# Performance work log

Hardware: AMD Instinct MI355X
Metric: run time of the kernel (lower is better)

Reference implementation:

```python
import jax, jax.numpy as jnp
import numpy as np
import math

B, S, E = 16, 600, 300   # batch, seq_len, enc_len
H, NC = 512, 2           # hidden, classes
D = S * E                # archi[0] = 180000


def setup_inputs() -> dict:
    key = jax.random.key(0)
    ks = jax.random.split(key, 7)
    x = jax.random.normal(ks[0], (B, S, E), dtype=jnp.float32)
    y = jax.random.randint(ks[1], (B,), 0, NC)
    # neurons initialized to zeros (init_neurons)
    n0 = jnp.zeros((B, S, E), jnp.float32)
    n1 = jnp.zeros((B, H), jnp.float32)
    n2 = jnp.zeros((B, NC), jnp.float32)
    # Linear weights (torch layout: [out, in]), Kaiming-uniform-like scale 1/sqrt(fan_in)
    W0 = jax.random.uniform(ks[2], (E, E), jnp.float32, -1.0, 1.0) / math.sqrt(E)
    W1 = jax.random.uniform(ks[3], (H, D), jnp.float32, -1.0, 1.0) / math.sqrt(D)
    b1 = jax.random.uniform(ks[4], (H,), jnp.float32, -1.0, 1.0) / math.sqrt(D)
    W2 = jax.random.uniform(ks[5], (NC, H), jnp.float32, -1.0, 1.0) / math.sqrt(H)
    b2 = jax.random.uniform(ks[6], (NC,), jnp.float32, -1.0, 1.0) / math.sqrt(H)
    return dict(x=x, y=y, n0=n0, n1=n1, n2=n2, W0=W0, W1=W1, b1=b1, W2=W2, b2=b2, T=3)


def reference(x, y, n0, n1, n2, W0, W1, b1, W2, b2, T):
    # EqProp free-phase relaxation (beta = 0.0, forward default).
    # Analytic dPhi/dneurons replaces torch.autograd.grad:
    scale = 1.0 / math.sqrt(E)
    Wx = jnp.einsum('bse,fe->bsf', x, W0)  # synapses[0](x), constant across steps
    for _ in range(T):
        g0 = Wx + (n1 @ W1).reshape(B, S, E)              # dPhi/dn0
        g1 = n0.reshape(B, D) @ W1.T + b1 + n2 @ W2       # dPhi/dn1
        g2 = n1 @ W2.T + b2                               # dPhi/dn2 (beta=0)
        # hand-coded attention update for neuron 0: Q=g0, K=V=x
        attn = jax.nn.softmax(scale * jnp.einsum('bse,bte->bst', g0, x), axis=-1)
        n0 = jnp.einsum('bst,bte->bse', attn, x)
        n1 = jnp.tanh(g1)
        n2 = jnp.tanh(g2)
    return n0, n1, n2
```

## Files before the change

kernel.cpp:

```cpp
#include <hip/hip_runtime.h>
#include <math.h>

#define DD 180000L
#define HH 512
#define BB 16
#define SS 600
#define EE 300
#define SP 608
#define EP 320

typedef unsigned short u16;
typedef __attribute__((ext_vector_type(8))) __bf16 bf16x8;
typedef __attribute__((ext_vector_type(4))) float f32x4;

__device__ __forceinline__ u16 f2bf(float f) {
  union { float f; unsigned int u; } x; x.f = f;
  unsigned int r = (x.u + 0x7FFFu + ((x.u >> 16) & 1u)) >> 16;
  return (u16)r;
}

__global__ __launch_bounds__(256) void k_conv_x(const float* __restrict__ x,
                                                u16* __restrict__ xb, u16* __restrict__ xt) {
  __shared__ u16 tl[32][33];
  int b = blockIdx.z;
  int tt = blockIdx.x * 32, ee = blockIdx.y * 32;
  int lx = threadIdx.x & 31, ly = threadIdx.x >> 5;
#pragma unroll
  for (int i = 0; i < 4; ++i) {
    int t = tt + ly + i * 8, e = ee + lx;
    float v = (t < SS && e < EE) ? x[((long)b * SS + t) * EE + e] : 0.f;
    u16 h = f2bf(v);
    xb[((long)b * SP + t) * EP + e] = h;
    tl[ly + i * 8][lx] = h;
  }
  __syncthreads();
#pragma unroll
  for (int i = 0; i < 4; ++i) {
    int e = ee + ly + i * 8, t = tt + lx;
    xt[((long)b * EP + e) * SP + t] = tl[lx][ly + i * 8];
  }
}

__global__ __launch_bounds__(256) void k_conv_w0(const float* __restrict__ W0, u16* __restrict__ w0b) {
  int idx = blockIdx.x * 256 + threadIdx.x;
  int f = idx / EP, e = idx % EP;
  float v = (f < EE && e < EE) ? W0[f * EE + e] : 0.f;
  w0b[idx] = f2bf(v);
}

__global__ __launch_bounds__(256) void k_gemm_nt(
    const u16* __restrict__ A, int lda, long sA, int Arows,
    const u16* __restrict__ B, int ldb, long sB, int Brows,
    float* __restrict__ C, int ldc, long sC, int Mv, int Nv, int K,
    u16* __restrict__ Cb, int ldcb, long sCb) {
  int bz = blockIdx.z;
  int m0 = blockIdx.x * 64, n0 = blockIdx.y * 64;
  int lane = threadIdx.x & 63, wv = threadIdx.x >> 6;
  int wm = m0 + (wv >> 1) * 32, wn = n0 + (wv & 1) * 32;
  int q = lane >> 4, ln = lane & 15;
  const u16* Ab = A + (long)bz * sA;
  const u16* Bb = B + (long)bz * sB;
  long arow0 = (long)min(wm + ln, Arows - 1) * lda;
  long arow1 = (long)min(wm + 16 + ln, Arows - 1) * lda;
  long brow0 = (long)min(wn + ln, Brows - 1) * ldb;
  long brow1 = (long)min(wn + 16 + ln, Brows - 1) * ldb;
  f32x4 acc00 = {0.f,0.f,0.f,0.f}, acc01 = acc00, acc10 = acc00, acc11 = acc00;
  int ksteps = (K + 31) >> 5;
  for (int kk = 0; kk < ksteps; ++kk) {
    int k0 = kk * 32 + q * 8;
    bf16x8 a0 = *(const bf16x8*)(Ab + arow0 + k0);
    bf16x8 a1 = *(const bf16x8*)(Ab + arow1 + k0);
    bf16x8 b0 = *(const bf16x8*)(Bb + brow0 + k0);
    bf16x8 bv1 = *(const bf16x8*)(Bb + brow1 + k0);
    acc00 = __builtin_amdgcn_mfma_f32_16x16x32_bf16(a0, b0,  acc00, 0, 0, 0);
    acc01 = __builtin_amdgcn_mfma_f32_16x16x32_bf16(a0, bv1, acc01, 0, 0, 0);
    acc10 = __builtin_amdgcn_mfma_f32_16x16x32_bf16(a1, b0,  acc10, 0, 0, 0);
    acc11 = __builtin_amdgcn_mfma_f32_16x16x32_bf16(a1, bv1, acc11, 0, 0, 0);
  }
  float* Cp = C + (long)bz * sC;
  u16* Cbp = Cb ? (Cb + (long)bz * sCb) : (u16*)0;
#pragma unroll
  for (int sm = 0; sm < 2; ++sm) {
#pragma unroll
    for (int sn = 0; sn < 2; ++sn) {
      f32x4 acc = (sm == 0) ? ((sn == 0) ? acc00 : acc01) : ((sn == 0) ? acc10 : acc11);
#pragma unroll
      for (int r = 0; r < 4; ++r) {
        int m = wm + sm * 16 + q * 4 + r;
        int n = wn + sn * 16 + ln;
        if (m < Mv && n < Nv) {
          float v = acc[r];
          Cp[(long)m * ldc + n] = v;
          if (Cbp) Cbp[(long)m * ldcb + n] = f2bf(v);
        }
      }
    }
  }
}

#define BN 256
#define BK 64
#define NCH 704

__global__ __launch_bounds__(256) void k_fused_w1(
    const float* __restrict__ W1, const float* __restrict__ n1f,
    const float* __restrict__ n0f, const float* __restrict__ Wx,
    u16* __restrict__ g0b, float* __restrict__ part) {
  __shared__ u16 wt[BK][BN + 8];
  __shared__ u16 n1s[BB][HH + 8];
  __shared__ u16 n0s[BB][BN + 8];
  int tid = threadIdx.x;
  long d0 = (long)blockIdx.x * BN;
#pragma unroll
  for (int i = 0; i < 8; ++i) {
    int f = i * 256 + tid;
    int b = f >> 7, c = (f & 127) * 4;
    float4 v = *(const float4*)(n1f + b * HH + c);
    n1s[b][c] = f2bf(v.x); n1s[b][c + 1] = f2bf(v.y);
    n1s[b][c + 2] = f2bf(v.z); n1s[b][c + 3] = f2bf(v.w);
  }
#pragma unroll
  for (int i = 0; i < 4; ++i) {
    int f = i * 256 + tid;
    int b = f >> 6, c = (f & 63) * 4;
    long d = d0 + c;
    float4 v = {0.f,0.f,0.f,0.f};
    if (d < DD) v = *(const float4*)(n0f + (long)b * DD + d);
    n0s[b][c] = f2bf(v.x); n0s[b][c + 1] = f2bf(v.y);
    n0s[b][c + 2] = f2bf(v.z); n0s[b][c + 3] = f2bf(v.w);
  }
  int lane = tid & 63, wv = tid >> 6, q = lane >> 4, ln = lane & 15;
  f32x4 acc0[4] = {{0.f,0.f,0.f,0.f},{0.f,0.f,0.f,0.f},{0.f,0.f,0.f,0.f},{0.f,0.f,0.f,0.f}};
  for (int s = 0; s < 8; ++s) {
    int h0 = s * BK;
    __syncthreads();
#pragma unroll
    for (int i = 0; i < 16; ++i) {
      int f = i * 256 + tid;
      int r = f >> 6, c = (f & 63) * 4;
      long d = d0 + c;
      float4 v = {0.f,0.f,0.f,0.f};
      if (d < DD) v = *(const float4*)(W1 + (long)(h0 + r) * DD + d);
      wt[r][c] = f2bf(v.x); wt[r][c + 1] = f2bf(v.y);
      wt[r][c + 2] = f2bf(v.z); wt[r][c + 3] = f2bf(v.w);
    }
    __syncthreads();
#pragma unroll
    for (int kst = 0; kst < 2; ++kst) {
      bf16x8 af = *(const bf16x8*)(&n1s[ln][h0 + kst * 32 + q * 8]);
#pragma unroll
      for (int nt = 0; nt < 4; ++nt) {
        int dc = wv * 64 + nt * 16 + ln;
        bf16x8 bv;
#pragma unroll
        for (int j = 0; j < 8; ++j) bv[j] = *(const __bf16*)(&wt[kst * 32 + q * 8 + j][dc]);
        acc0[nt] = __builtin_amdgcn_mfma_f32_16x16x32_bf16(af, bv, acc0[nt], 0, 0, 0);
      }
    }
    f32x4 acc1 = {0.f,0.f,0.f,0.f};
#pragma unroll
    for (int kst = 0; kst < 8; ++kst) {
      bf16x8 af = *(const bf16x8*)(&n0s[ln][kst * 32 + q * 8]);
      bf16x8 bv = *(const bf16x8*)(&wt[wv * 16 + ln][kst * 32 + q * 8]);
      acc1 = __builtin_amdgcn_mfma_f32_16x16x32_bf16(af, bv, acc1, 0, 0, 0);
    }
    long pb = (long)blockIdx.x * 8192;
#pragma unroll
    for (int r = 0; r < 4; ++r) {
      int b = q * 4 + r, h = h0 + wv * 16 + ln;
      part[pb + b * HH + h] = acc1[r];
    }
  }
#pragma unroll
  for (int nt = 0; nt < 4; ++nt) {
#pragma unroll
    for (int r = 0; r < 4; ++r) {
      int b = q * 4 + r;
      long d = d0 + wv * 64 + nt * 16 + ln;
      if (d < DD) {
        float val = Wx[(long)b * DD + d] + acc0[nt][r];
        int sI = (int)(d / EE), e = (int)(d % EE);
        g0b[((long)b * SS + sI) * EP + e] = f2bf(val);
      }
    }
  }
}

__global__ __launch_bounds__(256) void k_softmax(const float* __restrict__ S,
                                                 u16* __restrict__ P, float scale) {
  int s = blockIdx.x, b = blockIdx.y;
  const float* row = S + ((long)b * SP + s) * SP;
  u16* prow = P + ((long)b * SP + s) * SP;
  int tid = threadIdx.x, lane = tid & 63, wv = tid >> 6;
  __shared__ float red[8];
  float v[3]; float mx = -1e30f;
#pragma unroll
  for (int i = 0; i < 3; ++i) {
    int c = tid + i * 256;
    v[i] = (c < SS) ? row[c] * scale : -1e30f;
    mx = fmaxf(mx, v[i]);
  }
  for (int off = 32; off; off >>= 1) mx = fmaxf(mx, __shfl_down(mx, off));
  if (lane == 0) red[wv] = mx;
  __syncthreads();
  mx = fmaxf(fmaxf(red[0], red[1]), fmaxf(red[2], red[3]));
  float e[3], sum = 0.f;
#pragma unroll
  for (int i = 0; i < 3; ++i) {
    int c = tid + i * 256;
    e[i] = (c < SS) ? __expf(v[i] - mx) : 0.f;
    sum += e[i];
  }
  for (int off = 32; off; off >>= 1) sum += __shfl_down(sum, off);
  if (lane == 0) red[4 + wv] = sum;
  __syncthreads();
  float inv = 1.f / (red[4] + red[5] + red[6] + red[7]);
#pragma unroll
  for (int i = 0; i < 3; ++i) {
    int c = tid + i * 256;
    if (c < SS) prow[c] = f2bf(e[i] * inv);
  }
}

__global__ __launch_bounds__(256) void k_init(const float* __restrict__ b1, const float* __restrict__ b2,
                                              float* __restrict__ n1, float* __restrict__ n2) {
  int idx = blockIdx.x * 256 + threadIdx.x;
  n1[idx] = tanhf(b1[idx & 511]);
  if (idx < 32) n2[idx] = tanhf(b2[idx & 1]);
}

__global__ __launch_bounds__(64) void k_g2(const float* __restrict__ n1old, const float* __restrict__ W2,
                                           const float* __restrict__ b2, float* __restrict__ n2out) {
  int b = blockIdx.x >> 1, c = blockIdx.x & 1, lane = threadIdx.x;
  float s = 0.f;
#pragma unroll
  for (int i = 0; i < 8; ++i) { int h = lane + i * 64; s += n1old[b * HH + h] * W2[c * HH + h]; }
  for (int off = 32; off; off >>= 1) s += __shfl_down(s, off);
  if (lane == 0) n2out[b * 2 + c] = tanhf(s + b2[c]);
}

__global__ __launch_bounds__(256) void k_reduce1(const float* __restrict__ part, float* __restrict__ part2) {
  int idx = blockIdx.x * 256 + threadIdx.x;
  int sl = blockIdx.y;
  float s = 0.f;
  int c0 = sl * 88;
#pragma unroll 4
  for (int c = 0; c < 88; ++c) s += part[(long)(c0 + c) * 8192 + idx];
  part2[(long)sl * 8192 + idx] = s;
}

__global__ __launch_bounds__(256) void k_reduce2(const float* __restrict__ part2, const float* __restrict__ b1,
                                                 const float* __restrict__ W2, const float* __restrict__ n2old,
                                                 float* __restrict__ n1out) {
  int idx = blockIdx.x * 256 + threadIdx.x;
  int b = idx >> 9, h = idx & 511;
  float s = b1[h] + n2old[b * 2] * W2[h] + n2old[b * 2 + 1] * W2[HH + h];
#pragma unroll
  for (int sl = 0; sl < 8; ++sl) s += part2[(long)sl * 8192 + idx];
  n1out[idx] = tanhf(s);
}

extern "C" void kernel_launch(void* const* d_in, const int* in_sizes, int n_in,
                              void* d_out, int out_size, void* d_ws, size_t ws_size,
                              hipStream_t stream) {
  const float* x  = (const float*)d_in[0];
  const float* W0 = (const float*)d_in[5];
  const float* W1 = (const float*)d_in[6];
  const float* b1 = (const float*)d_in[7];
  const float* W2 = (const float*)d_in[8];
  const float* b2 = (const float*)d_in[9];

  float* out_n0 = (float*)d_out;
  float* out_n1 = out_n0 + 16L * SS * EE;
  float* out_n2 = out_n1 + 16L * HH;

  char* w = (char*)d_ws;
  auto take = [&](size_t bytes) { char* p = w; w += (bytes + 255) & ~(size_t)255; return p; };
  u16*   xb    = (u16*)take(16L * SP * EP * 2);
  u16*   xt    = (u16*)take(16L * EP * SP * 2);
  u16*   w0b   = (u16*)take((size_t)EP * EP * 2);
  float* Wx    = (float*)take(16L * SS * EE * 4);
  u16*   g0b   = (u16*)take(16L * SS * EP * 2);
  float* Sb    = (float*)take(16L * SP * SP * 4);
  u16*   attn  = (u16*)take(16L * SP * SP * 2);
  float* part2 = (float*)take(8L * 8192 * 4);
  float* n1A   = (float*)take(8192 * 4);
  float* n1B   = (float*)take(8192 * 4);
  float* n2A   = (float*)take(256);
  float* n2B   = (float*)take(256);
  float* part  = Sb;

  const float scale = 1.0f / sqrtf((float)EE);

  k_conv_x<<<dim3(19, 10, 16), 256, 0, stream>>>(x, xb, xt);
  k_conv_w0<<<400, 256, 0, stream>>>(W0, w0b);
  k_gemm_nt<<<dim3(10, 5, 16), 256, 0, stream>>>(xb, EP, (long)SP * EP, SP,
                                                 w0b, EP, 0, EP,
                                                 Wx, EE, (long)SS * EE, SS, EE, EE,
                                                 g0b, EP, (long)SS * EP);
  k_init<<<32, 256, 0, stream>>>(b1, b2, n1A, n2A);

  for (int it = 0; it < 3; ++it) {
    if (it > 0) {
      const float* n1old = (it == 1) ? n1A : n1B;
      const float* n2old = (it == 1) ? n2A : n2B;
      float* n2new = (it == 1) ? n2B : out_n2;
      float* n1new = (it == 1) ? n1B : out_n1;
      k_g2<<<32, 64, 0, stream>>>(n1old, W2, b2, n2new);
      k_fused_w1<<<NCH, 256, 0, stream>>>(W1, n1old, out_n0, Wx, g0b, part);
      k_reduce1<<<dim3(32, 8), 256, 0, stream>>>(part, part2);
      k_reduce2<<<32, 256, 0, stream>>>(part2, b1, W2, n2old, n1new);
    }
    k_gemm_nt<<<dim3(10, 10, 16), 256, 0, stream>>>(g0b, EP, (long)SS * EP, SS,
                                                    xb, EP, (long)SP * EP, SP,
                                                    Sb, SP, (long)SP * SP, SP, SP, EE,
                                                    (u16*)0, 0, 0);
    k_softmax<<<dim3(SS, 16), 256, 0, stream>>>(Sb, attn, scale);
    k_gemm_nt<<<dim3(10, 5, 16), 256, 0, stream>>>(attn, SP, (long)SP * SP, SP,
                                                   xt, SP, (long)EP * SP, EP,
                                                   out_n0, EE, (long)DD, SS, EE, SP,
                                                   (u16*)0, 0, 0);
  }
}
```

Before: 972.1 us.

## Fuse score GEMM, softmax and PV GEMM into one attention kernel; prefetch W1 tiles

Replaces the three-kernel attention sequence (score GEMM to a global fp32 buffer, softmax to a bf16 buffer, PV GEMM) with a single kernel per 16-query tile. It computes scores with MFMA, keeps them in shared memory, applies softmax, and multiplies by V, which removes the large intermediate global round-trips and two launches per iteration. The fused W1 kernel also register-prefetches the next W1 chunk before the current one is consumed, to overlap global loads with compute. The GEMM epilogue now zero-fills the padded bf16 columns of g0b, so the new kernel does not read garbage. The fused attention kernel uses only 38x16 blocks, each with large shared memory, so occupancy and the repeated K/V reads from global memory are risks.

```diff
diff --git a/kernel.cpp b/kernel.cpp
--- a/kernel.cpp
+++ b/kernel.cpp
@@ -88,10 +88,10 @@
       for (int r = 0; r < 4; ++r) {
         int m = wm + sm * 16 + q * 4 + r;
         int n = wn + sn * 16 + ln;
-        if (m < Mv && n < Nv) {
+        if (m < Mv) {
           float v = acc[r];
-          Cp[(long)m * ldc + n] = v;
-          if (Cbp) Cbp[(long)m * ldcb + n] = f2bf(v);
+          if (n < Nv) Cp[(long)m * ldc + n] = v;
+          if (Cbp && n < ldcb) Cbp[(long)m * ldcb + n] = f2bf(n < Nv ? v : 0.f);
         }
       }
     }
@@ -131,6 +131,17 @@
   }
   int lane = tid & 63, wv = tid >> 6, q = lane >> 4, ln = lane & 15;
   f32x4 acc0[4] = {{0.f,0.f,0.f,0.f},{0.f,0.f,0.f,0.f},{0.f,0.f,0.f,0.f},{0.f,0.f,0.f,0.f}};
+
+  float4 pre[16];
+#pragma unroll
+  for (int i = 0; i < 16; ++i) {
+    int f = i * 256 + tid;
+    int r = f >> 6, c = (f & 63) * 4;
+    long d = d0 + c;
+    float4 v = {0.f,0.f,0.f,0.f};
+    if (d < DD) v = *(const float4*)(W1 + (long)r * DD + d);
+    pre[i] = v;
+  }
   for (int s = 0; s < 8; ++s) {
     int h0 = s * BK;
     __syncthreads();
@@ -138,11 +149,19 @@
     for (int i = 0; i < 16; ++i) {
       int f = i * 256 + tid;
       int r = f >> 6, c = (f & 63) * 4;
-      long d = d0 + c;
-      float4 v = {0.f,0.f,0.f,0.f};
-      if (d < DD) v = *(const float4*)(W1 + (long)(h0 + r) * DD + d);
-      wt[r][c] = f2bf(v.x); wt[r][c + 1] = f2bf(v.y);
-      wt[r][c + 2] = f2bf(v.z); wt[r][c + 3] = f2bf(v.w);
+      wt[r][c] = f2bf(pre[i].x); wt[r][c + 1] = f2bf(pre[i].y);
+      wt[r][c + 2] = f2bf(pre[i].z); wt[r][c + 3] = f2bf(pre[i].w);
+    }
+    if (s < 7) {
+#pragma unroll
+      for (int i = 0; i < 16; ++i) {
+        int f = i * 256 + tid;
+        int r = f >> 6, c = (f & 63) * 4;
+        long d = d0 + c;
+        float4 v = {0.f,0.f,0.f,0.f};
+        if (d < DD) v = *(const float4*)(W1 + (long)(h0 + BK + r) * DD + d);
+        pre[i] = v;
+      }
     }
     __syncthreads();
 #pragma unroll
@@ -186,39 +205,107 @@
   }
 }
 
-__global__ __launch_bounds__(256) void k_softmax(const float* __restrict__ S,
-                                                 u16* __restrict__ P, float scale) {
-  int s = blockIdx.x, b = blockIdx.y;
-  const float* row = S + ((long)b * SP + s) * SP;
-  u16* prow = P + ((long)b * SP + s) * SP;
-  int tid = threadIdx.x, lane = tid & 63, wv = tid >> 6;
-  __shared__ float red[8];
-  float v[3]; float mx = -1e30f;
+__global__ __launch_bounds__(256) void k_flash(const u16* __restrict__ g0b,
+                                               const u16* __restrict__ xb,
+                                               const u16* __restrict__ xt,
+                                               float* __restrict__ out_n0, float scale) {
+  __shared__ u16 Qs[16][328];
+  __shared__ float Ss[16][609];
+  __shared__ u16 Ps[16][616];
+  int qt = blockIdx.x, b = blockIdx.y;
+  int tid = threadIdx.x, lane = tid & 63, wv = tid >> 6, q = lane >> 4, ln = lane & 15;
+
 #pragma unroll
   for (int i = 0; i < 3; ++i) {
     int c = tid + i * 256;
-    v[i] = (c < SS) ? row[c] * scale : -1e30f;
-    mx = fmaxf(mx, v[i]);
-  }
-  for (int off = 32; off; off >>= 1) mx = fmaxf(mx, __shfl_down(mx, off));
-  if (lane == 0) red[wv] = mx;
+    if (c < 640) {
+      int row = c / 40, cg = (c % 40) * 8;
+      int qrow = min(qt * 16 + row, SS - 1);
+      bf16x8 v = *(const bf16x8*)(g0b + ((long)b * SS + qrow) * EP + cg);
+#pragma unroll
+      for (int j = 0; j < 8; ++j) if (cg + j >= EE) v[j] = (__bf16)0.f;
+      *(bf16x8*)&Qs[row][cg] = v;
+    }
+  }
   __syncthreads();
-  mx = fmaxf(fmaxf(red[0], red[1]), fmaxf(red[2], red[3]));
-  float e[3], sum = 0.f;
-#pragma unroll
-  for (int i = 0; i < 3; ++i) {
-    int c = tid + i * 256;
-    e[i] = (c < SS) ? __expf(v[i] - mx) : 0.f;
-    sum += e[i];
-  }
-  for (int off = 32; off; off >>= 1) sum += __shfl_down(sum, off);
-  if (lane == 0) red[4 + wv] = sum;
+
+  f32x4 sacc[10];
+#pragma unroll
+  for (int i = 0; i < 10; ++i) sacc[i] = (f32x4){0.f,0.f,0.f,0.f};
+  for (int k = 0; k < 10; ++k) {
+    bf16x8 af = *(const bf16x8*)&Qs[ln][k * 32 + q * 8];
+#pragma unroll
+    for (int nt = 0; nt < 10; ++nt) {
+      int tile = nt * 4 + wv;
+      if (tile < 38) {
+        bf16x8 bv = *(const bf16x8*)(xb + ((long)b * SP + tile * 16 + ln) * EP + k * 32 + q * 8);
+        sacc[nt] = __builtin_amdgcn_mfma_f32_16x16x32_bf16(af, bv, sacc[nt], 0, 0, 0);
+      }
+    }
+  }
+#pragma unroll
+  for (int nt = 0; nt < 10; ++nt) {
+    int tile = nt * 4 + wv;
+    if (tile < 38) {
+#pragma unroll
+      for (int r = 0; r < 4; ++r)
+        Ss[q * 4 + r][tile * 16 + ln] = sacc[nt][r] * scale;
+    }
+  }
   __syncthreads();
-  float inv = 1.f / (red[4] + red[5] + red[6] + red[7]);
-#pragma unroll
-  for (int i = 0; i < 3; ++i) {
-    int c = tid + i * 256;
-    if (c < SS) prow[c] = f2bf(e[i] * inv);
+
+#pragma unroll
+  for (int r = 0; r < 4; ++r) {
+    int row = wv * 4 + r;
+    float v[10], mx = -1e30f;
+#pragma unroll
+    for (int i = 0; i < 10; ++i) {
+      int c = lane + i * 64;
+      v[i] = (c < SS) ? Ss[row][c] : -1e30f;
+      mx = fmaxf(mx, v[i]);
+    }
+#pragma unroll
+    for (int off = 1; off < 64; off <<= 1) mx = fmaxf(mx, __shfl_xor(mx, off));
+    float sum = 0.f;
+#pragma unroll
+    for (int i = 0; i < 10; ++i) {
+      int c = lane + i * 64;
+      v[i] = (c < SS) ? __expf(v[i] - mx) : 0.f;
+      sum += v[i];
+    }
+#pragma unroll
+    for (int off = 1; off < 64; off <<= 1) sum += __shfl_xor(sum, off);
+    float inv = 1.f / sum;
+#pragma unroll
+    for (int i = 0; i < 10; ++i) {
+      int c = lane + i * 64;
+      if (c < SP) Ps[row][c] = f2bf(v[i] * inv);
+    }
+  }
+  __syncthreads();
+
+  f32x4 oacc[5];
+#pragma unroll
+  for (int j = 0; j < 5; ++j) oacc[j] = (f32x4){0.f,0.f,0.f,0.f};
+  for (int k = 0; k < 19; ++k) {
+    bf16x8 af = *(const bf16x8*)&Ps[ln][k * 32 + q * 8];
+#pragma unroll
+    for (int j = 0; j < 5; ++j) {
+      int e = (j * 4 + wv) * 16 + ln;
+      bf16x8 bv = *(const bf16x8*)(xt + ((long)b * EP + e) * SP + k * 32 + q * 8);
+      oacc[j] = __builtin_amdgcn_mfma_f32_16x16x32_bf16(af, bv, oacc[j], 0, 0, 0);
+    }
+  }
+#pragma unroll
+  for (int j = 0; j < 5; ++j) {
+    int e = (j * 4 + wv) * 16 + ln;
+    if (e < EE) {
+#pragma unroll
+      for (int r = 0; r < 4; ++r) {
+        int qrow = qt * 16 + q * 4 + r;
+        if (qrow < SS) out_n0[((long)b * SS + qrow) * EE + e] = oacc[j][r];
+      }
+    }
   }
 }
 
@@ -281,14 +368,12 @@
   u16*   w0b   = (u16*)take((size_t)EP * EP * 2);
   float* Wx    = (float*)take(16L * SS * EE * 4);
   u16*   g0b   = (u16*)take(16L * SS * EP * 2);
-  float* Sb    = (float*)take(16L * SP * SP * 4);
-  u16*   attn  = (u16*)take(16L * SP * SP * 2);
+  float* part  = (float*)take((size_t)NCH * 8192 * 4);
   float* part2 = (float*)take(8L * 8192 * 4);
   float* n1A   = (float*)take(8192 * 4);
   float* n1B   = (float*)take(8192 * 4);
   float* n2A   = (float*)take(256);
   float* n2B   = (float*)take(256);
-  float* part  = Sb;
 
   const float scale = 1.0f / sqrtf((float)EE);
 
@@ -311,14 +396,6 @@
       k_reduce1<<<dim3(32, 8), 256, 0, stream>>>(part, part2);
       k_reduce2<<<32, 256, 0, stream>>>(part2, b1, W2, n2old, n1new);
     }
-    k_gemm_nt<<<dim3(10, 10, 16), 256, 0, stream>>>(g0b, EP, (long)SS * EP, SS,
-                                                    xb, EP, (long)SP * EP, SP,
-                                                    Sb, SP, (long)SP * SP, SP, SP, EE,
-                                                    (u16*)0, 0, 0);
-    k_softmax<<<dim3(SS, 16), 256, 0, stream>>>(Sb, attn, scale);
-    k_gemm_nt<<<dim3(10, 5, 16), 256, 0, stream>>>(attn, SP, (long)SP * SP, SP,
-                                                   xt, SP, (long)EP * SP, EP,
-                                                   out_n0, EE, (long)DD, SS, EE, SP,
-                                                   (u16*)0, 0, 0);
-  }
-}
+    k_flash<<<dim3(38, 16), 256, 0, stream>>>(g0b, xb, xt, out_n0, scale);
+  }
+}
```

Result: no change. 974.9 us (+0.3%).
